# Kernel optimization log

Hardware: AMD Instinct MI355X
Metric: run time of the kernel (lower is better)

The kernel has to match this reference:

```python
import jax, jax.numpy as jnp
import numpy as np

N = 20000
E = 320000
IN_C = 256
OUT_C = 64
HEADS = 4
NEG_SLOPE = 0.2
HID = HEADS * OUT_C  # 256, layer-2 input width (concat=True)


def setup_inputs() -> dict:
    key = jax.random.key(0)
    ks = jax.random.split(key, 16)
    x = jax.random.normal(ks[0], (N, IN_C), dtype=jnp.float32)
    edge_index = jax.random.randint(ks[1], (2, E), 0, N, dtype=jnp.int32)

    def glorot(k, shape, fan_in):
        return jax.random.normal(k, shape, dtype=jnp.float32) * np.float32(1.0 / np.sqrt(fan_in))

    inp = {"x": x, "edge_index": edge_index}
    # two GATv2Conv layers, both in_dim=256 -> heads*out=256
    for li, kbase in ((1, 2), (2, 9)):
        in_dim = IN_C if li == 1 else HID
        inp[f"Wl{li}"] = glorot(ks[kbase + 0], (in_dim, HID), in_dim)
        inp[f"bl{li}"] = jnp.zeros((HID,), jnp.float32)
        inp[f"Wr{li}"] = glorot(ks[kbase + 1], (in_dim, HID), in_dim)
        inp[f"br{li}"] = jnp.zeros((HID,), jnp.float32)
        inp[f"att{li}"] = glorot(ks[kbase + 2], (HEADS, OUT_C), OUT_C)
        inp[f"bias{li}"] = jnp.zeros((HID,), jnp.float32)
    return inp


def _gatv2_layer(x, src, dst, Wl, bl, Wr, br, att, bias):
    # GATv2Conv (PyG semantics, eval mode so attention dropout is identity)
    xl = (x @ Wl + bl).reshape(N, HEADS, OUT_C)  # source transform
    xr = (x @ Wr + br).reshape(N, HEADS, OUT_C)  # target transform
    # per-edge attention logits: a^T LeakyReLU(xl_j + xr_i)
    e = jax.nn.leaky_relu(xl[src] + xr[dst], NEG_SLOPE)      # [E2, H, C]
    logits = jnp.einsum('ehc,hc->eh', e, att)                # [E2, H]
    # segment softmax over incoming edges of each target node
    m = jax.ops.segment_max(logits, dst, num_segments=N)      # [N, H]
    ex = jnp.exp(logits - m[dst])
    denom = jax.ops.segment_sum(ex, dst, num_segments=N)      # [N, H]
    alpha = ex / denom[dst]                                   # [E2, H]
    msg = xl[src] * alpha[:, :, None]                         # [E2, H, C]
    out = jax.ops.segment_sum(msg, dst, num_segments=N)       # [N, H, C]
    return out.reshape(N, HID) + bias


def reference(x, edge_index, Wl1, bl1, Wr1, br1, att1, bias1,
              Wl2, bl2, Wr2, br2, att2, bias2):
    # add self loops (PyG GATv2Conv default add_self_loops=True)
    loops = jnp.arange(N, dtype=edge_index.dtype)
    src = jnp.concatenate([edge_index[0], loops])
    dst = jnp.concatenate([edge_index[1], loops])
    h = _gatv2_layer(x, src, dst, Wl1, bl1, Wr1, br1, att1, bias1)
    h = jax.nn.relu(h)
    h = _gatv2_layer(h, src, dst, Wl2, bl2, Wr2, br2, att2, bias2)
    h = jax.nn.relu(h)
    return h
```

## Files before the change

### kernel.cpp

```cpp
#include <hip/hip_runtime.h>

#define N_NODES 20000
#define E_EDGES 320000
#define E2 (E_EDGES + N_NODES)
#define HID 256
#define SLOPE 0.2f

__global__ __launch_bounds__(256) void k_init(int* __restrict__ deg, int* __restrict__ cursor) {
    int i = blockIdx.x * 256 + threadIdx.x;
    if (i < N_NODES) { deg[i] = 1; cursor[i] = 0; }
}

__global__ __launch_bounds__(256) void k_degree(const int* __restrict__ dst, int* __restrict__ deg) {
    int e = blockIdx.x * 256 + threadIdx.x;
    if (e < E_EDGES) atomicAdd(&deg[dst[e]], 1);
}

__global__ __launch_bounds__(1024) void k_scan(const int* __restrict__ deg, int* __restrict__ off) {
    __shared__ int wsum[16];
    const int tid  = threadIdx.x;
    const int wave = tid >> 6;
    const int lane = tid & 63;
    int carry = 0;
    for (int base = 0; base < N_NODES; base += 1024) {
        const int i = base + tid;
        const int v = (i < N_NODES) ? deg[i] : 0;
        int x = v;
        #pragma unroll
        for (int o = 1; o < 64; o <<= 1) {
            int t = __shfl_up(x, o);
            if (lane >= o) x += t;
        }
        if (lane == 63) wsum[wave] = x;
        __syncthreads();
        if (wave == 0 && lane < 16) {
            int y = wsum[lane];
            #pragma unroll
            for (int o = 1; o < 16; o <<= 1) {
                int t = __shfl_up(y, o);
                if (lane >= o) y += t;
            }
            wsum[lane] = y;
        }
        __syncthreads();
        const int wbase = (wave == 0) ? 0 : wsum[wave - 1];
        if (i < N_NODES) off[i] = carry + wbase + (x - v);
        carry += wsum[15];
        __syncthreads();
    }
    if (tid == 0) off[N_NODES] = carry;
}

__global__ __launch_bounds__(256) void k_fill(const int* __restrict__ srcA, const int* __restrict__ dstA,
                                              const int* __restrict__ off, int* __restrict__ cursor,
                                              int* __restrict__ csr_src) {
    int e = blockIdx.x * 256 + threadIdx.x;
    if (e >= E2) return;
    int s, d;
    if (e < E_EDGES) { s = srcA[e]; d = dstA[e]; }
    else             { s = d = e - E_EDGES; }
    int pos = atomicAdd(&cursor[d], 1);
    csr_src[off[d] + pos] = s;
}

__global__ __launch_bounds__(256) void k_gemm(const float* __restrict__ X,
                                              const float* __restrict__ Wl, const float* __restrict__ Wr,
                                              const float* __restrict__ bl, const float* __restrict__ br,
                                              float* __restrict__ xl, float* __restrict__ xr) {
    __shared__ float As[32][132];
    __shared__ float Bs[32][68];
    const int tid = threadIdx.x;
    const int m0  = blockIdx.x * 128;
    const int by  = blockIdx.y;
    const float* W    = (by < 4) ? Wl : Wr;
    const float* bias = (by < 4) ? bl : br;
    float*       C    = (by < 4) ? xl : xr;
    const int n0 = (by & 3) * 64;
    const int tx = tid & 15;
    const int ty = tid >> 4;
    const int ar = tid >> 3;
    const int ac = (tid & 7) * 4;
    const int bkr = tid >> 4;
    const int bcc = (tid & 15) * 4;

    float acc[8][4] = {};
    for (int k0 = 0; k0 < 256; k0 += 32) {
        float4 av[4], bv[2];
        #pragma unroll
        for (int i = 0; i < 4; ++i) {
            const int gm = m0 + ar + i * 32;
            av[i] = (gm < N_NODES)
                ? *(const float4*)&X[(size_t)gm * 256 + k0 + ac]
                : make_float4(0.f, 0.f, 0.f, 0.f);
        }
        #pragma unroll
        for (int i = 0; i < 2; ++i)
            bv[i] = *(const float4*)&W[(size_t)(k0 + bkr + i * 16) * 256 + n0 + bcc];

        __syncthreads();
        #pragma unroll
        for (int i = 0; i < 4; ++i) {
            const int mm = ar + i * 32;
            As[ac + 0][mm] = av[i].x;
            As[ac + 1][mm] = av[i].y;
            As[ac + 2][mm] = av[i].z;
            As[ac + 3][mm] = av[i].w;
        }
        #pragma unroll
        for (int i = 0; i < 2; ++i)
            *(float4*)&Bs[bkr + i * 16][bcc] = bv[i];
        __syncthreads();

        #pragma unroll
        for (int kk = 0; kk < 32; ++kk) {
            float a8[8], b4[4];
            *(float4*)&a8[0] = *(const float4*)&As[kk][ty * 4];
            *(float4*)&a8[4] = *(const float4*)&As[kk][ty * 4 + 64];
            *(float4*)&b4[0] = *(const float4*)&Bs[kk][tx * 4];
            #pragma unroll
            for (int i = 0; i < 8; ++i)
                #pragma unroll
                for (int j = 0; j < 4; ++j)
                    acc[i][j] = fmaf(a8[i], b4[j], acc[i][j]);
        }
    }

    float4 bb4 = *(const float4*)&bias[n0 + tx * 4];
    float bb[4] = {bb4.x, bb4.y, bb4.z, bb4.w};
    #pragma unroll
    for (int half = 0; half < 2; ++half) {
        #pragma unroll
        for (int i = 0; i < 4; ++i) {
            const int gm = m0 + half * 64 + ty * 4 + i;
            if (gm < N_NODES) {
                const int ai = half * 4 + i;
                float4 o;
                o.x = acc[ai][0] + bb[0];
                o.y = acc[ai][1] + bb[1];
                o.z = acc[ai][2] + bb[2];
                o.w = acc[ai][3] + bb[3];
                *(float4*)&C[(size_t)gm * 256 + n0 + tx * 4] = o;
            }
        }
    }
}

__global__ __launch_bounds__(256) void k_edge(const float* __restrict__ xl, const float* __restrict__ xr,
                                              const float* __restrict__ att,
                                              const int* __restrict__ csr_src, const int* __restrict__ off,
                                              const float* __restrict__ bias,
                                              float* __restrict__ out) {
    const int node = (blockIdx.x * 256 + threadIdx.x) >> 6;
    const int l = threadIdx.x & 63;
    if (node >= N_NODES) return;

    const float4 w  = *(const float4*)&att[l * 4];
    const float4 xd = *(const float4*)&xr[(size_t)node * 256 + l * 4];
    const int beg = off[node], end = off[node + 1];

    float m = -1e30f, ssum = 0.f;
    float4 acc = make_float4(0.f, 0.f, 0.f, 0.f);

    int j1 = csr_src[beg];
    float4 a_nxt = *(const float4*)&xl[(size_t)j1 * 256 + l * 4];
    int j2 = (beg + 1 < end) ? csr_src[beg + 1] : 0;

    for (int p = beg; p < end; ++p) {
        const float4 a = a_nxt;
        if (p + 1 < end)
            a_nxt = *(const float4*)&xl[(size_t)j2 * 256 + l * 4];
        if (p + 2 < end)
            j2 = csr_src[p + 2];

        float t = 0.f, u;
        u = a.x + xd.x; u = (u > 0.f) ? u : SLOPE * u; t = fmaf(u, w.x, t);
        u = a.y + xd.y; u = (u > 0.f) ? u : SLOPE * u; t = fmaf(u, w.y, t);
        u = a.z + xd.z; u = (u > 0.f) ? u : SLOPE * u; t = fmaf(u, w.z, t);
        u = a.w + xd.w; u = (u > 0.f) ? u : SLOPE * u; t = fmaf(u, w.w, t);
        t += __shfl_xor(t, 1);
        t += __shfl_xor(t, 2);
        t += __shfl_xor(t, 4);
        t += __shfl_xor(t, 8);

        const float nm = fmaxf(m, t);
        const float sc = __expf(m - nm);
        const float wp = __expf(t - nm);
        acc.x = fmaf(acc.x, sc, wp * a.x);
        acc.y = fmaf(acc.y, sc, wp * a.y);
        acc.z = fmaf(acc.z, sc, wp * a.z);
        acc.w = fmaf(acc.w, sc, wp * a.w);
        ssum  = fmaf(ssum, sc, wp);
        m = nm;
    }
    const float inv = 1.0f / ssum;
    const float4 bv = *(const float4*)&bias[l * 4];
    float4 o;
    o.x = fmaxf(fmaf(acc.x, inv, bv.x), 0.f);
    o.y = fmaxf(fmaf(acc.y, inv, bv.y), 0.f);
    o.z = fmaxf(fmaf(acc.z, inv, bv.z), 0.f);
    o.w = fmaxf(fmaf(acc.w, inv, bv.w), 0.f);
    *(float4*)&out[(size_t)node * 256 + l * 4] = o;
}

extern "C" void kernel_launch(void* const* d_in, const int* in_sizes, int n_in,
                              void* d_out, int out_size, void* d_ws, size_t ws_size,
                              hipStream_t stream) {
    const float* x    = (const float*)d_in[0];
    const int*   ei   = (const int*)d_in[1];
    const float* Wl1  = (const float*)d_in[2];
    const float* bl1  = (const float*)d_in[3];
    const float* Wr1  = (const float*)d_in[4];
    const float* br1  = (const float*)d_in[5];
    const float* att1 = (const float*)d_in[6];
    const float* bias1= (const float*)d_in[7];
    const float* Wl2  = (const float*)d_in[8];
    const float* bl2  = (const float*)d_in[9];
    const float* Wr2  = (const float*)d_in[10];
    const float* br2  = (const float*)d_in[11];
    const float* att2 = (const float*)d_in[12];
    const float* bias2= (const float*)d_in[13];
    float* out = (float*)d_out;

    const int* src = ei;
    const int* dst = ei + E_EDGES;

    char* ws = (char*)d_ws;
    size_t o = 0;
    auto alloc = [&](size_t bytes) -> void* {
        void* p = ws + o;
        o += (bytes + 255) & ~(size_t)255;
        return p;
    };
    float* xl      = (float*)alloc((size_t)N_NODES * HID * 4);
    float* xr      = (float*)alloc((size_t)N_NODES * HID * 4);
    float* hbuf    = (float*)alloc((size_t)N_NODES * HID * 4);
    int*   csr_src = (int*)alloc((size_t)E2 * 4);
    int*   off     = (int*)alloc((size_t)(N_NODES + 1) * 4);
    int*   deg     = (int*)alloc((size_t)N_NODES * 4);
    int*   cursor  = (int*)alloc((size_t)N_NODES * 4);
    (void)ws_size; (void)n_in; (void)in_sizes; (void)out_size;

    k_init<<<(N_NODES + 255) / 256, 256, 0, stream>>>(deg, cursor);
    k_degree<<<(E_EDGES + 255) / 256, 256, 0, stream>>>(dst, deg);
    k_scan<<<1, 1024, 0, stream>>>(deg, off);
    k_fill<<<(E2 + 255) / 256, 256, 0, stream>>>(src, dst, off, cursor, csr_src);

    dim3 ggrid((N_NODES + 127) / 128, 8);

    k_gemm<<<ggrid, 256, 0, stream>>>(x, Wl1, Wr1, bl1, br1, xl, xr);
    k_edge<<<(N_NODES * 64 + 255) / 256, 256, 0, stream>>>(xl, xr, att1, csr_src, off, bias1, hbuf);

    k_gemm<<<ggrid, 256, 0, stream>>>(hbuf, Wl2, Wr2, bl2, br2, xl, xr);
    k_edge<<<(N_NODES * 64 + 255) / 256, 256, 0, stream>>>(xl, xr, att2, csr_src, off, bias2, out);
}
```

Before: 399.2 us.

## Replace FP32 SIMT GEMM with split-bf16 MFMA GEMM (3-term hi/lo emulation)

Replaces the shared-memory FP32 FMA GEMM with a matrix-core GEMM using bf16 MFMA 16x16x32. Operands are split into bf16 hi and lo parts and combined as three products to keep near-FP32 accuracy. Weights are converted and transposed once per call, x is converted by a new kernel, and the layer-1 edge kernel now writes its output directly as hi/lo bf16 pairs for layer 2. The aim is to move the dense transform onto matrix cores. The cost is extra conversion kernels, more MFMA work from the three-term scheme, and fragment loads straight from global memory with no LDS reuse.

```diff
diff --git a/kernel.cpp b/kernel.cpp
--- a/kernel.cpp
+++ b/kernel.cpp
@@ -5,6 +5,23 @@
 #define E2 (E_EDGES + N_NODES)
 #define HID 256
 #define SLOPE 0.2f
+
+typedef __bf16 bf16x8 __attribute__((ext_vector_type(8)));
+typedef float  f32x4  __attribute__((ext_vector_type(4)));
+typedef unsigned int uint4v __attribute__((ext_vector_type(4)));
+
+__device__ __forceinline__ unsigned short f2bf(float f) {
+    unsigned b = __float_as_uint(f);
+    return (unsigned short)((b + 0x7FFFu + ((b >> 16) & 1u)) >> 16);
+}
+__device__ __forceinline__ float bf2f(unsigned short h) {
+    return __uint_as_float(((unsigned)h) << 16);
+}
+__device__ __forceinline__ bf16x8 ld_frag(const unsigned short* p) {
+    uint4v u = *reinterpret_cast<const uint4v*>(p);
+    return __builtin_bit_cast(bf16x8, u);
+}
+#define MFMA16(a, b, c) __builtin_amdgcn_mfma_f32_16x16x32_bf16((a), (b), (c), 0, 0, 0)
 
 __global__ __launch_bounds__(256) void k_init(int* __restrict__ deg, int* __restrict__ cursor) {
     int i = blockIdx.x * 256 + threadIdx.x;
@@ -63,93 +80,112 @@
     csr_src[off[d] + pos] = s;
 }
 
-__global__ __launch_bounds__(256) void k_gemm(const float* __restrict__ X,
-                                              const float* __restrict__ Wl, const float* __restrict__ Wr,
-                                              const float* __restrict__ bl, const float* __restrict__ br,
-                                              float* __restrict__ xl, float* __restrict__ xr) {
-    __shared__ float As[32][132];
-    __shared__ float Bs[32][68];
-    const int tid = threadIdx.x;
-    const int m0  = blockIdx.x * 128;
-    const int by  = blockIdx.y;
-    const float* W    = (by < 4) ? Wl : Wr;
+__global__ __launch_bounds__(256) void k_cvt_x(const float* __restrict__ X,
+                                               unsigned short* __restrict__ hi,
+                                               unsigned short* __restrict__ lo) {
+    const int i = blockIdx.x * 256 + threadIdx.x;
+    if (i >= N_NODES * HID / 4) return;
+    float4 v = ((const float4*)X)[i];
+    ushort4 h, l;
+    h.x = f2bf(v.x); l.x = f2bf(v.x - bf2f(h.x));
+    h.y = f2bf(v.y); l.y = f2bf(v.y - bf2f(h.y));
+    h.z = f2bf(v.z); l.z = f2bf(v.z - bf2f(h.z));
+    h.w = f2bf(v.w); l.w = f2bf(v.w - bf2f(h.w));
+    ((ushort4*)hi)[i] = h;
+    ((ushort4*)lo)[i] = l;
+}
+
+__global__ __launch_bounds__(256) void k_cvt_w(const float* __restrict__ W0, const float* __restrict__ W1,
+                                               const float* __restrict__ W2, const float* __restrict__ W3,
+                                               unsigned short* __restrict__ wt_hi,
+                                               unsigned short* __restrict__ wt_lo) {
+    const float* W = (blockIdx.x == 0) ? W0 : (blockIdx.x == 1) ? W1 : (blockIdx.x == 2) ? W2 : W3;
+    unsigned short* oh = wt_hi + (size_t)blockIdx.x * 65536;
+    unsigned short* ol = wt_lo + (size_t)blockIdx.x * 65536;
+    const int n = threadIdx.x;
+    const int k0 = blockIdx.y * 16;
+    for (int k = k0; k < k0 + 16; ++k) {
+        float v = W[(size_t)k * 256 + n];
+        unsigned short h = f2bf(v);
+        oh[(size_t)n * 256 + k] = h;
+        ol[(size_t)n * 256 + k] = f2bf(v - bf2f(h));
+    }
+}
+
+__global__ __launch_bounds__(256) void k_gemm_mfma(
+        const unsigned short* __restrict__ Ahi, const unsigned short* __restrict__ Alo,
+        const unsigned short* __restrict__ WhiL, const unsigned short* __restrict__ WloL,
+        const unsigned short* __restrict__ WhiR, const unsigned short* __restrict__ WloR,
+        const float* __restrict__ bl, const float* __restrict__ br,
+        float* __restrict__ xl, float* __restrict__ xr) {
+    const int tid  = threadIdx.x;
+    const int lane = tid & 63;
+    const int wave = tid >> 6;
+    const int m0   = blockIdx.x * 128 + wave * 32;
+    const int by   = blockIdx.y;
+    const unsigned short* Whi = (by < 4) ? WhiL : WhiR;
+    const unsigned short* Wlo = (by < 4) ? WloL : WloR;
     const float* bias = (by < 4) ? bl : br;
     float*       C    = (by < 4) ? xl : xr;
     const int n0 = (by & 3) * 64;
-    const int tx = tid & 15;
-    const int ty = tid >> 4;
-    const int ar = tid >> 3;
-    const int ac = (tid & 7) * 4;
-    const int bkr = tid >> 4;
-    const int bcc = (tid & 15) * 4;
-
-    float acc[8][4] = {};
+
+    const int lrow = lane & 15;
+    const int lkb  = lane >> 4;
+    int ar0 = m0 + lrow;       ar0 = (ar0 < N_NODES) ? ar0 : N_NODES - 1;
+    int ar1 = m0 + 16 + lrow;  ar1 = (ar1 < N_NODES) ? ar1 : N_NODES - 1;
+    const size_t aoff0 = (size_t)ar0 * HID + lkb * 8;
+    const size_t aoff1 = (size_t)ar1 * HID + lkb * 8;
+
+    f32x4 acc[2][4];
+    #pragma unroll
+    for (int i = 0; i < 2; ++i)
+        #pragma unroll
+        for (int j = 0; j < 4; ++j)
+            acc[i][j] = (f32x4){0.f, 0.f, 0.f, 0.f};
+
     for (int k0 = 0; k0 < 256; k0 += 32) {
-        float4 av[4], bv[2];
+        const bf16x8 a0h = ld_frag(Ahi + aoff0 + k0);
+        const bf16x8 a0l = ld_frag(Alo + aoff0 + k0);
+        const bf16x8 a1h = ld_frag(Ahi + aoff1 + k0);
+        const bf16x8 a1l = ld_frag(Alo + aoff1 + k0);
         #pragma unroll
-        for (int i = 0; i < 4; ++i) {
-            const int gm = m0 + ar + i * 32;
-            av[i] = (gm < N_NODES)
-                ? *(const float4*)&X[(size_t)gm * 256 + k0 + ac]
-                : make_float4(0.f, 0.f, 0.f, 0.f);
+        for (int ct = 0; ct < 4; ++ct) {
+            const size_t boff = (size_t)(n0 + ct * 16 + lrow) * HID + k0 + lkb * 8;
+            const bf16x8 bh = ld_frag(Whi + boff);
+            const bf16x8 bw = ld_frag(Wlo + boff);
+            acc[0][ct] = MFMA16(a0h, bh, acc[0][ct]);
+            acc[0][ct] = MFMA16(a0h, bw, acc[0][ct]);
+            acc[0][ct] = MFMA16(a0l, bh, acc[0][ct]);
+            acc[1][ct] = MFMA16(a1h, bh, acc[1][ct]);
+            acc[1][ct] = MFMA16(a1h, bw, acc[1][ct]);
+            acc[1][ct] = MFMA16(a1l, bh, acc[1][ct]);
         }
+    }
+
+    #pragma unroll
+    for (int ct = 0; ct < 4; ++ct) {
+        const int gcol = n0 + ct * 16 + lrow;
+        const float bb = bias[gcol];
         #pragma unroll
-        for (int i = 0; i < 2; ++i)
-            bv[i] = *(const float4*)&W[(size_t)(k0 + bkr + i * 16) * 256 + n0 + bcc];
-
-        __syncthreads();
-        #pragma unroll
-        for (int i = 0; i < 4; ++i) {
-            const int mm = ar + i * 32;
-            As[ac + 0][mm] = av[i].x;
-            As[ac + 1][mm] = av[i].y;
-            As[ac + 2][mm] = av[i].z;
-            As[ac + 3][mm] = av[i].w;
-        }
-        #pragma unroll
-        for (int i = 0; i < 2; ++i)
-            *(float4*)&Bs[bkr + i * 16][bcc] = bv[i];
-        __syncthreads();
-
-        #pragma unroll
-        for (int kk = 0; kk < 32; ++kk) {
-            float a8[8], b4[4];
-            *(float4*)&a8[0] = *(const float4*)&As[kk][ty * 4];
-            *(float4*)&a8[4] = *(const float4*)&As[kk][ty * 4 + 64];
-            *(float4*)&b4[0] = *(const float4*)&Bs[kk][tx * 4];
+        for (int rt = 0; rt < 2; ++rt) {
             #pragma unroll
-            for (int i = 0; i < 8; ++i)
-                #pragma unroll
-                for (int j = 0; j < 4; ++j)
-                    acc[i][j] = fmaf(a8[i], b4[j], acc[i][j]);
-        }
-    }
-
-    float4 bb4 = *(const float4*)&bias[n0 + tx * 4];
-    float bb[4] = {bb4.x, bb4.y, bb4.z, bb4.w};
-    #pragma unroll
-    for (int half = 0; half < 2; ++half) {
-        #pragma unroll
-        for (int i = 0; i < 4; ++i) {
-            const int gm = m0 + half * 64 + ty * 4 + i;
-            if (gm < N_NODES) {
-                const int ai = half * 4 + i;
-                float4 o;
-                o.x = acc[ai][0] + bb[0];
-                o.y = acc[ai][1] + bb[1];
-                o.z = acc[ai][2] + bb[2];
-                o.w = acc[ai][3] + bb[3];
-                *(float4*)&C[(size_t)gm * 256 + n0 + tx * 4] = o;
+            for (int j = 0; j < 4; ++j) {
+                const int grow = m0 + rt * 16 + lkb * 4 + j;
+                if (grow < N_NODES)
+                    C[(size_t)grow * HID + gcol] = acc[rt][ct][j] + bb;
             }
         }
     }
 }
 
+template <bool FP32OUT>
 __global__ __launch_bounds__(256) void k_edge(const float* __restrict__ xl, const float* __restrict__ xr,
                                               const float* __restrict__ att,
                                               const int* __restrict__ csr_src, const int* __restrict__ off,
                                               const float* __restrict__ bias,
-                                              float* __restrict__ out) {
+                                              float* __restrict__ outF,
+                                              unsigned short* __restrict__ outHi,
+                                              unsigned short* __restrict__ outLo) {
     const int node = (blockIdx.x * 256 + threadIdx.x) >> 6;
     const int l = threadIdx.x & 63;
     if (node >= N_NODES) return;
@@ -199,7 +235,17 @@
     o.y = fmaxf(fmaf(acc.y, inv, bv.y), 0.f);
     o.z = fmaxf(fmaf(acc.z, inv, bv.z), 0.f);
     o.w = fmaxf(fmaf(acc.w, inv, bv.w), 0.f);
-    *(float4*)&out[(size_t)node * 256 + l * 4] = o;
+    if (FP32OUT) {
+        *(float4*)&outF[(size_t)node * 256 + l * 4] = o;
+    } else {
+        ushort4 h, lo;
+        h.x = f2bf(o.x); lo.x = f2bf(o.x - bf2f(h.x));
+        h.y = f2bf(o.y); lo.y = f2bf(o.y - bf2f(h.y));
+        h.z = f2bf(o.z); lo.z = f2bf(o.z - bf2f(h.z));
+        h.w = f2bf(o.w); lo.w = f2bf(o.w - bf2f(h.w));
+        *(ushort4*)&outHi[(size_t)node * 256 + l * 4] = h;
+        *(ushort4*)&outLo[(size_t)node * 256 + l * 4] = lo;
+    }
 }
 
 extern "C" void kernel_launch(void* const* d_in, const int* in_sizes, int n_in,
@@ -231,13 +277,16 @@
         o += (bytes + 255) & ~(size_t)255;
         return p;
     };
-    float* xl      = (float*)alloc((size_t)N_NODES * HID * 4);
-    float* xr      = (float*)alloc((size_t)N_NODES * HID * 4);
-    float* hbuf    = (float*)alloc((size_t)N_NODES * HID * 4);
-    int*   csr_src = (int*)alloc((size_t)E2 * 4);
-    int*   off     = (int*)alloc((size_t)(N_NODES + 1) * 4);
-    int*   deg     = (int*)alloc((size_t)N_NODES * 4);
-    int*   cursor  = (int*)alloc((size_t)N_NODES * 4);
+    float*          xl      = (float*)alloc((size_t)N_NODES * HID * 4);
+    float*          xr      = (float*)alloc((size_t)N_NODES * HID * 4);
+    unsigned short* bufA_hi = (unsigned short*)alloc((size_t)N_NODES * HID * 2);
+    unsigned short* bufA_lo = (unsigned short*)alloc((size_t)N_NODES * HID * 2);
+    unsigned short* wt_hi   = (unsigned short*)alloc((size_t)4 * 65536 * 2);
+    unsigned short* wt_lo   = (unsigned short*)alloc((size_t)4 * 65536 * 2);
+    int*            csr_src = (int*)alloc((size_t)E2 * 4);
+    int*            off     = (int*)alloc((size_t)(N_NODES + 1) * 4);
+    int*            deg     = (int*)alloc((size_t)N_NODES * 4);
+    int*            cursor  = (int*)alloc((size_t)N_NODES * 4);
     (void)ws_size; (void)n_in; (void)in_sizes; (void)out_size;
 
     k_init<<<(N_NODES + 255) / 256, 256, 0, stream>>>(deg, cursor);
@@ -245,11 +294,22 @@
     k_scan<<<1, 1024, 0, stream>>>(deg, off);
     k_fill<<<(E2 + 255) / 256, 256, 0, stream>>>(src, dst, off, cursor, csr_src);
 
+    k_cvt_w<<<dim3(4, 16), 256, 0, stream>>>(Wl1, Wr1, Wl2, Wr2, wt_hi, wt_lo);
+    k_cvt_x<<<(N_NODES * HID / 4 + 255) / 256, 256, 0, stream>>>(x, bufA_hi, bufA_lo);
+
     dim3 ggrid((N_NODES + 127) / 128, 8);
-
-    k_gemm<<<ggrid, 256, 0, stream>>>(x, Wl1, Wr1, bl1, br1, xl, xr);
-    k_edge<<<(N_NODES * 64 + 255) / 256, 256, 0, stream>>>(xl, xr, att1, csr_src, off, bias1, hbuf);
-
-    k_gemm<<<ggrid, 256, 0, stream>>>(hbuf, Wl2, Wr2, bl2, br2, xl, xr);
-    k_edge<<<(N_NODES * 64 + 255) / 256, 256, 0, stream>>>(xl, xr, att2, csr_src, off, bias2, out);
-}
+    const int egrid = (N_NODES * 64 + 255) / 256;
+
+    k_gemm_mfma<<<ggrid, 256, 0, stream>>>(bufA_hi, bufA_lo,
+                                           wt_hi, wt_lo, wt_hi + 65536, wt_lo + 65536,
+                                           bl1, br1, xl, xr);
+    k_edge<false><<<egrid, 256, 0, stream>>>(xl, xr, att1, csr_src, off, bias1,
+                                             nullptr, bufA_hi, bufA_lo);
+
+    k_gemm_mfma<<<ggrid, 256, 0, stream>>>(bufA_hi, bufA_lo,
+                                           wt_hi + 2 * 65536, wt_lo + 2 * 65536,
+                                           wt_hi + 3 * 65536, wt_lo + 3 * 65536,
+                                           bl2, br2, xl, xr);
+    k_edge<true><<<egrid, 256, 0, stream>>>(xl, xr, att2, csr_src, off, bias2,
+                                            out, nullptr, nullptr);
+}
```

New measurement: 405.8 us. No clear change (+1.7%).
